# Optimization experiments

Hardware: AMD Instinct MI355X
Metric: run time of the kernel (lower is better)

Reference implementation:

```python
import jax, jax.numpy as jnp
import numpy as np

WS = 8                       # window size (square)
N = WS * WS                  # tokens per window
RES_H, RES_W = 32, 32        # input_resolution
DIM = 512
NUM_HEADS = 16
HEAD_DIM = DIM // NUM_HEADS
SCALE = HEAD_DIM ** -0.5
TABLE = 2 * WS - 1           # size of a_p/b_p/a_r/b_r tables
B_ = 1024                    # num_windows * batch


def _rel_coords():
    c = np.arange(WS)
    coords = np.stack(np.meshgrid(c, c, indexing='ij'))          # (2, WS, WS)
    cf = coords.reshape(2, -1)                                   # (2, N)
    rel = cf[:, :, None] - cf[:, None, :]                        # (2, N, N), values in [-(WS-1), WS-1]
    return rel[0], rel[1]                                        # radius (dh), azimuth (dw)

RADIUS_NP, AZIMUTH_NP = _rel_coords()
# torch indexes the (2*WS-1)-row tables with negative indices -> python wrap: -k maps to TABLE-k
IDX_R = jnp.asarray(RADIUS_NP % TABLE)
IDX_AZ = jnp.asarray(AZIMUTH_NP % TABLE)
RADIUS = jnp.asarray(RADIUS_NP, dtype=jnp.float32)               # (N, N)
AZIMUTH = jnp.asarray(AZIMUTH_NP, dtype=jnp.float32)             # (N, N)


def setup_inputs() -> dict:
    key = jax.random.key(0)
    ks = jax.random.split(key, 10)
    return {
        'x': jax.random.normal(ks[0], (B_, N, DIM), dtype=jnp.float32),
        'theta_max': jnp.ones((), dtype=jnp.float32) * 1.5708,   # ~pi/2 field-of-view half-angle
        'qkv_w': jax.random.normal(ks[1], (3 * DIM, DIM), dtype=jnp.float32) * 0.02,
        'qkv_b': jnp.zeros((3 * DIM,), dtype=jnp.float32),
        'proj_w': jax.random.normal(ks[2], (DIM, DIM), dtype=jnp.float32) * 0.02,
        'proj_b': jnp.zeros((DIM,), dtype=jnp.float32),
        'a_p': jax.random.normal(ks[3], (TABLE, NUM_HEADS), dtype=jnp.float32) * 0.02,
        'b_p': jax.random.normal(ks[4], (TABLE, NUM_HEADS), dtype=jnp.float32) * 0.02,
        'a_r': jax.random.normal(ks[5], (TABLE, NUM_HEADS), dtype=jnp.float32) * 0.02,
        'b_r': jax.random.normal(ks[6], (TABLE, NUM_HEADS), dtype=jnp.float32) * 0.02,
    }


def _trig_bias(table_a, table_b, idx, angle):
    # table_[ab]: (TABLE, H); idx: (N, N) int; angle: (N, N) float (possibly traced)
    a = table_a[idx]                                              # (N, N, H)
    b = table_b[idx]
    ang = angle[:, :, None]                                       # (N, N, 1)
    bias = a * jnp.cos(ang) + b * jnp.sin(ang)                    # (N, N, H)
    return jnp.transpose(bias, (2, 0, 1))                         # (H, N, N)


def reference(x, theta_max, qkv_w, qkv_b, proj_w, proj_b, a_p, b_p, a_r, b_r):
    Bw, n, c = x.shape
    qkv = x @ qkv_w.T + qkv_b                                     # (B_, N, 3*DIM)
    qkv = qkv.reshape(Bw, n, 3, NUM_HEADS, HEAD_DIM)
    qkv = jnp.transpose(qkv, (2, 0, 3, 1, 4))                     # (3, B_, H, N, hd)
    q, k, v = qkv[0] * SCALE, qkv[1], qkv[2]

    attn = jnp.einsum('bhid,bhjd->bhij', q, k)                    # (B_, H, N, N)

    az_angle = AZIMUTH * (2.0 * np.pi / RES_W)                    # (N, N)
    A_phi = _trig_bias(a_p, b_p, IDX_AZ, az_angle)                # (H, N, N)
    r_angle = RADIUS * (theta_max / RES_H)                        # (N, N), traced via theta_max
    A_theta = _trig_bias(a_r, b_r, IDX_R, r_angle)                # (H, N, N)

    attn = attn + A_phi[None] + A_theta[None]
    attn = jax.nn.softmax(attn, axis=-1)

    out = jnp.einsum('bhij,bhjd->bhid', attn, v)                  # (B_, H, N, hd)
    out = jnp.transpose(out, (0, 2, 1, 3)).reshape(Bw, n, c)      # (B_, N, DIM)
    out = out @ proj_w.T + proj_b
    return out
```

## Files before the change

### kernel.cpp

```cpp
#include <hip/hip_runtime.h>
#include <hip/hip_bf16.h>


typedef __bf16 bf16_t;
typedef bf16_t bf16x8 __attribute__((ext_vector_type(8)));
typedef float  f32x4  __attribute__((ext_vector_type(4)));

#define NWIN   1024
#define NTOK   64
#define DIM    512
#define NHEADS 16
#define HD     32
#define MTOT   (NWIN*NTOK)
#define QKVN   (3*DIM)
#define SCALE  0.17677669529663687f

__device__ __forceinline__ void async_copy16(const void* g, void* lds_generic) {
    __builtin_amdgcn_global_load_lds(
        (__attribute__((address_space(1))) unsigned int*)(unsigned long long)g,
        (__attribute__((address_space(3))) unsigned int*)(unsigned int)(unsigned long long)lds_generic,
        16, 0, 0);
}

__global__ void cvt_f32_bf16(const float* __restrict__ in, bf16_t* __restrict__ out, int n8) {
    int i = blockIdx.x * blockDim.x + threadIdx.x;
    if (i >= n8) return;
    const float4* p = (const float4*)in;
    float4 a = p[2*i], b = p[2*i+1];
    bf16x8 o;
    o[0]=(bf16_t)a.x; o[1]=(bf16_t)a.y; o[2]=(bf16_t)a.z; o[3]=(bf16_t)a.w;
    o[4]=(bf16_t)b.x; o[5]=(bf16_t)b.y; o[6]=(bf16_t)b.z; o[7]=(bf16_t)b.w;
    ((bf16x8*)out)[i] = o;
}

__global__ void bias_kernel(const float* __restrict__ ap, const float* __restrict__ bp,
                            const float* __restrict__ ar, const float* __restrict__ br,
                            const float* __restrict__ theta_max, float* __restrict__ bias) {
    int idx = blockIdx.x * 256 + threadIdx.x;
    int h  = idx >> 12;
    int ij = idx & 4095;
    int i = ij >> 6, j = ij & 63;
    int ri = i >> 3, ci = i & 7, rj = j >> 3, cj = j & 7;
    int rad = ri - rj, az = ci - cj;
    int idx_r  = rad < 0 ? rad + 15 : rad;
    int idx_az = az  < 0 ? az  + 15 : az;
    float azang = (float)az * 0.19634954084936207f;
    float rang  = (float)rad * (theta_max[0] * (1.0f/32.0f));
    float v = ap[idx_az*NHEADS + h] * cosf(azang) + bp[idx_az*NHEADS + h] * sinf(azang)
            + ar[idx_r *NHEADS + h] * cosf(rang)  + br[idx_r *NHEADS + h] * sinf(rang);
    bias[idx] = v;
}

template<int OUT_BF16>
__global__ __launch_bounds__(256, 2)
void gemm_bt(const bf16_t* __restrict__ A, const bf16_t* __restrict__ Bt,
             const float* __restrict__ bias, void* __restrict__ C,
             int M, int N, int K, int ntiles) {
    __shared__ bf16_t sA[128*64];
    __shared__ bf16_t sB[128*64];

    int bid = blockIdx.x;
    int bm = bid / ntiles, bn = bid % ntiles;
    int tid = threadIdx.x;
    int w = tid >> 6, lane = tid & 63;
    int quad = lane >> 4, l16 = lane & 15;
    int wm = w >> 1, wn = w & 1;

    f32x4 acc[4][4] = {};

    const bf16_t* Abase = A  + (size_t)(bm*128) * K;
    const bf16_t* Bbase = Bt + (size_t)(bn*128) * K;

    for (int k0 = 0; k0 < K; k0 += 64) {
        for (int i = 0; i < 4; ++i) {
            int off = w*4096 + i*1024 + lane*16;
            int r  = off >> 7;
            int pb = (off >> 4) & 7;
            int cb = pb ^ (r & 7);
            async_copy16(Abase + (size_t)r*K + k0 + cb*8, (char*)sA + w*4096 + i*1024);
            async_copy16(Bbase + (size_t)r*K + k0 + cb*8, (char*)sB + w*4096 + i*1024);
        }
        __syncthreads();

        for (int kk = 0; kk < 64; kk += 32) {
            bf16x8 af[4], bf[4];
            for (int mi = 0; mi < 4; ++mi) {
                int r  = wm*64 + mi*16 + l16;
                int cb = (kk >> 3) + quad;
                int pb = cb ^ (r & 7);
                af[mi] = *(const bf16x8*)((const char*)sA + r*128 + pb*16);
            }
            for (int ni = 0; ni < 4; ++ni) {
                int r  = wn*64 + ni*16 + l16;
                int cb = (kk >> 3) + quad;
                int pb = cb ^ (r & 7);
                bf[ni] = *(const bf16x8*)((const char*)sB + r*128 + pb*16);
            }
            for (int mi = 0; mi < 4; ++mi)
                for (int ni = 0; ni < 4; ++ni)
                    acc[mi][ni] = __builtin_amdgcn_mfma_f32_16x16x32_bf16(
                        af[mi], bf[ni], acc[mi][ni], 0, 0, 0);
        }
        __syncthreads();
    }

    for (int ni = 0; ni < 4; ++ni) {
        int col = bn*128 + wn*64 + ni*16 + l16;
        float bv = bias[col];
        for (int mi = 0; mi < 4; ++mi) {
            int row0 = bm*128 + wm*64 + mi*16 + quad*4;
            f32x4 a = acc[mi][ni];
            for (int reg = 0; reg < 4; ++reg) {
                float v = a[reg] + bv;
                size_t o = (size_t)(row0 + reg) * N + col;
                if (OUT_BF16) ((bf16_t*)C)[o] = (bf16_t)v;
                else          ((float*)C)[o]  = v;
            }
        }
    }
}

__global__ __launch_bounds__(256)
void attn_kernel(const bf16_t* __restrict__ qkv, const float* __restrict__ bias,
                 bf16_t* __restrict__ h2) {
    __shared__ bf16_t P[64*72];
    __shared__ bf16_t vT[32*64];

    int b = blockIdx.x >> 4, h = blockIdx.x & 15;
    int tid = threadIdx.x;
    int w = tid >> 6, lane = tid & 63, quad = lane >> 4, l16 = lane & 15;
    const bf16_t* base = qkv + (size_t)(b*64) * QKVN;

    {
        int t = tid & 63, dg = tid >> 6;
        bf16x8 vv = *(const bf16x8*)(base + (size_t)t*QKVN + 1024 + h*32 + dg*8);
        for (int j = 0; j < 8; ++j) vT[(dg*8 + j)*64 + t] = vv[j];
    }

    int m0 = w * 16;
    bf16x8 aq = *(const bf16x8*)(base + (size_t)(m0 + l16)*QKVN + h*32 + quad*8);
    f32x4 zero = {0.f, 0.f, 0.f, 0.f};
    f32x4 accS[4];
    for (int jt = 0; jt < 4; ++jt) {
        bf16x8 bk = *(const bf16x8*)(base + (size_t)(jt*16 + l16)*QKVN + 512 + h*32 + quad*8);
        accS[jt] = __builtin_amdgcn_mfma_f32_16x16x32_bf16(aq, bk, zero, 0, 0, 0);
    }

    const float* bh = bias + h*4096;
    float p[4][4], inv[4];
    for (int reg = 0; reg < 4; ++reg) {
        int row = m0 + quad*4 + reg;
        for (int jt = 0; jt < 4; ++jt)
            p[jt][reg] = accS[jt][reg] * SCALE + bh[row*64 + jt*16 + l16];
        float m = fmaxf(fmaxf(p[0][reg], p[1][reg]), fmaxf(p[2][reg], p[3][reg]));
        for (int off = 1; off < 16; off <<= 1) m = fmaxf(m, __shfl_xor(m, off));
        float s = 0.f;
        for (int jt = 0; jt < 4; ++jt) { p[jt][reg] = __expf(p[jt][reg] - m); s += p[jt][reg]; }
        for (int off = 1; off < 16; off <<= 1) s += __shfl_xor(s, off);
        inv[reg] = 1.0f / s;
    }
    for (int reg = 0; reg < 4; ++reg) {
        int row = m0 + quad*4 + reg;
        for (int jt = 0; jt < 4; ++jt)
            P[row*72 + jt*16 + l16] = (bf16_t)p[jt][reg];
    }
    __syncthreads();

    f32x4 accO[2] = {zero, zero};
    for (int kb = 0; kb < 64; kb += 32) {
        bf16x8 ap = *(const bf16x8*)(&P[(m0 + l16)*72 + kb + quad*8]);
        for (int nt = 0; nt < 2; ++nt) {
            bf16x8 bv = *(const bf16x8*)(&vT[(nt*16 + l16)*64 + kb + quad*8]);
            accO[nt] = __builtin_amdgcn_mfma_f32_16x16x32_bf16(ap, bv, accO[nt], 0, 0, 0);
        }
    }
    for (int nt = 0; nt < 2; ++nt) {
        for (int reg = 0; reg < 4; ++reg) {
            int row = b*64 + m0 + quad*4 + reg;
            int col = h*32 + nt*16 + l16;
            h2[(size_t)row*DIM + col] = (bf16_t)(accO[nt][reg] * inv[reg]);
        }
    }
}

extern "C" void kernel_launch(void* const* d_in, const int* in_sizes, int n_in,
                              void* d_out, int out_size, void* d_ws, size_t ws_size,
                              hipStream_t stream) {
    const float* x      = (const float*)d_in[0];
    const float* theta  = (const float*)d_in[1];
    const float* qkv_w  = (const float*)d_in[2];
    const float* qkv_b  = (const float*)d_in[3];
    const float* proj_w = (const float*)d_in[4];
    const float* proj_b = (const float*)d_in[5];
    const float* a_p    = (const float*)d_in[6];
    const float* b_p    = (const float*)d_in[7];
    const float* a_r    = (const float*)d_in[8];
    const float* b_r    = (const float*)d_in[9];
    float* out = (float*)d_out;

    char* ws = (char*)d_ws;
    bf16_t* qkvbuf = (bf16_t*)ws;
    bf16_t* xb     = (bf16_t*)(ws + 201326592);
    bf16_t* h2     = (bf16_t*)(ws + 201326592 + 67108864);
    bf16_t* wqkv   = (bf16_t*)(ws + 201326592 + 2*67108864);
    bf16_t* wproj  = (bf16_t*)(ws + 201326592 + 2*67108864 + 1572864);
    float*  biasbf = (float*) (ws + 201326592 + 2*67108864 + 1572864 + 524288);

    cvt_f32_bf16<<<(MTOT*DIM/8)/256, 256, 0, stream>>>(x, xb, MTOT*DIM/8);
    cvt_f32_bf16<<<(QKVN*DIM/8)/256, 256, 0, stream>>>(qkv_w, wqkv, QKVN*DIM/8);
    cvt_f32_bf16<<<(DIM*DIM/8)/256, 256, 0, stream>>>(proj_w, wproj, DIM*DIM/8);

    bias_kernel<<<256, 256, 0, stream>>>(a_p, b_p, a_r, b_r, theta, biasbf);

    gemm_bt<1><<<(MTOT/128)*(QKVN/128), 256, 0, stream>>>(xb, wqkv, qkv_b, qkvbuf,
                                                          MTOT, QKVN, DIM, QKVN/128);
    attn_kernel<<<NWIN*NHEADS, 256, 0, stream>>>(qkvbuf, biasbf, h2);

    gemm_bt<0><<<(MTOT/128)*(DIM/128), 256, 0, stream>>>(h2, wproj, proj_b, out,
                                                         MTOT, DIM, DIM, DIM/128);
}
```

Baseline: 558.2 us.

## Fuse per-window attention over all heads with output projection in one kernel

Replaces the per-(window,head) attention kernel and the separate projection GEMM with a single kernel per window. It loops over all 16 heads, accumulates the concatenated head outputs in LDS, then multiplies by the projection weights read directly from global memory and adds the bias. This removes the bf16 intermediate h2 round trip and one launch, but there are only 1024 blocks, heads run serially with barriers, and the proj weights are reloaded from global/L2 by every block without LDS staging.

```diff
diff --git a/kernel.cpp b/kernel.cpp
--- a/kernel.cpp
+++ b/kernel.cpp
@@ -120,65 +120,92 @@
     }
 }
 
-__global__ __launch_bounds__(256)
-void attn_kernel(const bf16_t* __restrict__ qkv, const float* __restrict__ bias,
-                 bf16_t* __restrict__ h2) {
+__global__ __launch_bounds__(256, 2)
+void attn_proj_kernel(const bf16_t* __restrict__ qkv, const float* __restrict__ bias,
+                      const bf16_t* __restrict__ projw, const float* __restrict__ projb,
+                      float* __restrict__ out) {
+    __shared__ bf16_t aout[64*520];
     __shared__ bf16_t P[64*72];
-    __shared__ bf16_t vT[32*64];
-
-    int b = blockIdx.x >> 4, h = blockIdx.x & 15;
+    __shared__ bf16_t vT[32*72];
+
+    int b = blockIdx.x;
     int tid = threadIdx.x;
     int w = tid >> 6, lane = tid & 63, quad = lane >> 4, l16 = lane & 15;
     const bf16_t* base = qkv + (size_t)(b*64) * QKVN;
-
-    {
-        int t = tid & 63, dg = tid >> 6;
-        bf16x8 vv = *(const bf16x8*)(base + (size_t)t*QKVN + 1024 + h*32 + dg*8);
-        for (int j = 0; j < 8; ++j) vT[(dg*8 + j)*64 + t] = vv[j];
-    }
-
+    f32x4 zero = {0.f, 0.f, 0.f, 0.f};
     int m0 = w * 16;
-    bf16x8 aq = *(const bf16x8*)(base + (size_t)(m0 + l16)*QKVN + h*32 + quad*8);
-    f32x4 zero = {0.f, 0.f, 0.f, 0.f};
-    f32x4 accS[4];
-    for (int jt = 0; jt < 4; ++jt) {
-        bf16x8 bk = *(const bf16x8*)(base + (size_t)(jt*16 + l16)*QKVN + 512 + h*32 + quad*8);
-        accS[jt] = __builtin_amdgcn_mfma_f32_16x16x32_bf16(aq, bk, zero, 0, 0, 0);
-    }
-
-    const float* bh = bias + h*4096;
-    float p[4][4], inv[4];
-    for (int reg = 0; reg < 4; ++reg) {
-        int row = m0 + quad*4 + reg;
-        for (int jt = 0; jt < 4; ++jt)
-            p[jt][reg] = accS[jt][reg] * SCALE + bh[row*64 + jt*16 + l16];
-        float m = fmaxf(fmaxf(p[0][reg], p[1][reg]), fmaxf(p[2][reg], p[3][reg]));
-        for (int off = 1; off < 16; off <<= 1) m = fmaxf(m, __shfl_xor(m, off));
-        float s = 0.f;
-        for (int jt = 0; jt < 4; ++jt) { p[jt][reg] = __expf(p[jt][reg] - m); s += p[jt][reg]; }
-        for (int off = 1; off < 16; off <<= 1) s += __shfl_xor(s, off);
-        inv[reg] = 1.0f / s;
-    }
-    for (int reg = 0; reg < 4; ++reg) {
-        int row = m0 + quad*4 + reg;
-        for (int jt = 0; jt < 4; ++jt)
-            P[row*72 + jt*16 + l16] = (bf16_t)p[jt][reg];
-    }
-    __syncthreads();
-
-    f32x4 accO[2] = {zero, zero};
-    for (int kb = 0; kb < 64; kb += 32) {
-        bf16x8 ap = *(const bf16x8*)(&P[(m0 + l16)*72 + kb + quad*8]);
-        for (int nt = 0; nt < 2; ++nt) {
-            bf16x8 bv = *(const bf16x8*)(&vT[(nt*16 + l16)*64 + kb + quad*8]);
-            accO[nt] = __builtin_amdgcn_mfma_f32_16x16x32_bf16(ap, bv, accO[nt], 0, 0, 0);
-        }
-    }
-    for (int nt = 0; nt < 2; ++nt) {
+
+    for (int h = 0; h < NHEADS; ++h) {
+        {
+            int t = tid & 63, dg = tid >> 6;
+            bf16x8 vv = *(const bf16x8*)(base + (size_t)t*QKVN + 1024 + h*32 + dg*8);
+            for (int j = 0; j < 8; ++j) vT[(dg*8 + j)*72 + t] = vv[j];
+        }
+
+        bf16x8 aq = *(const bf16x8*)(base + (size_t)(m0 + l16)*QKVN + h*32 + quad*8);
+        f32x4 accS[4];
+        for (int jt = 0; jt < 4; ++jt) {
+            bf16x8 bk = *(const bf16x8*)(base + (size_t)(jt*16 + l16)*QKVN + 512 + h*32 + quad*8);
+            accS[jt] = __builtin_amdgcn_mfma_f32_16x16x32_bf16(aq, bk, zero, 0, 0, 0);
+        }
+
+        const float* bh = bias + h*4096;
+        float p[4][4], inv[4];
         for (int reg = 0; reg < 4; ++reg) {
-            int row = b*64 + m0 + quad*4 + reg;
-            int col = h*32 + nt*16 + l16;
-            h2[(size_t)row*DIM + col] = (bf16_t)(accO[nt][reg] * inv[reg]);
+            int row = m0 + quad*4 + reg;
+            for (int jt = 0; jt < 4; ++jt)
+                p[jt][reg] = accS[jt][reg] * SCALE + bh[row*64 + jt*16 + l16];
+            float m = fmaxf(fmaxf(p[0][reg], p[1][reg]), fmaxf(p[2][reg], p[3][reg]));
+            for (int off = 1; off < 16; off <<= 1) m = fmaxf(m, __shfl_xor(m, off));
+            float s = 0.f;
+            for (int jt = 0; jt < 4; ++jt) { p[jt][reg] = __expf(p[jt][reg] - m); s += p[jt][reg]; }
+            for (int off = 1; off < 16; off <<= 1) s += __shfl_xor(s, off);
+            inv[reg] = 1.0f / s;
+        }
+        for (int reg = 0; reg < 4; ++reg) {
+            int row = m0 + quad*4 + reg;
+            for (int jt = 0; jt < 4; ++jt)
+                P[row*72 + jt*16 + l16] = (bf16_t)p[jt][reg];
+        }
+        __syncthreads();
+
+        f32x4 accO[2] = {zero, zero};
+        for (int kb = 0; kb < 64; kb += 32) {
+            bf16x8 ap = *(const bf16x8*)(&P[(m0 + l16)*72 + kb + quad*8]);
+            for (int nt = 0; nt < 2; ++nt) {
+                bf16x8 bv = *(const bf16x8*)(&vT[(nt*16 + l16)*72 + kb + quad*8]);
+                accO[nt] = __builtin_amdgcn_mfma_f32_16x16x32_bf16(ap, bv, accO[nt], 0, 0, 0);
+            }
+        }
+        for (int nt = 0; nt < 2; ++nt)
+            for (int reg = 0; reg < 4; ++reg)
+                aout[(m0 + quad*4 + reg)*520 + h*32 + nt*16 + l16] =
+                    (bf16_t)(accO[nt][reg] * inv[reg]);
+        __syncthreads();
+    }
+
+    for (int half = 0; half < 2; ++half) {
+        f32x4 acc[4][4] = {};
+        for (int kk = 0; kk < 512; kk += 32) {
+            bf16x8 af[4], bfr[4];
+            for (int mi = 0; mi < 4; ++mi)
+                af[mi] = *(const bf16x8*)(&aout[(mi*16 + l16)*520 + kk + quad*8]);
+            for (int ni = 0; ni < 4; ++ni)
+                bfr[ni] = *(const bf16x8*)(projw + (size_t)(w*128 + half*64 + ni*16 + l16)*512 + kk + quad*8);
+            for (int mi = 0; mi < 4; ++mi)
+                for (int ni = 0; ni < 4; ++ni)
+                    acc[mi][ni] = __builtin_amdgcn_mfma_f32_16x16x32_bf16(
+                        af[mi], bfr[ni], acc[mi][ni], 0, 0, 0);
+        }
+        for (int ni = 0; ni < 4; ++ni) {
+            int col = w*128 + half*64 + ni*16 + l16;
+            float bv = projb[col];
+            for (int mi = 0; mi < 4; ++mi) {
+                int row0 = b*64 + mi*16 + quad*4;
+                f32x4 a = acc[mi][ni];
+                for (int reg = 0; reg < 4; ++reg)
+                    out[(size_t)(row0 + reg)*DIM + col] = a[reg] + bv;
+            }
         }
     }
 }
@@ -201,10 +228,9 @@
     char* ws = (char*)d_ws;
     bf16_t* qkvbuf = (bf16_t*)ws;
     bf16_t* xb     = (bf16_t*)(ws + 201326592);
-    bf16_t* h2     = (bf16_t*)(ws + 201326592 + 67108864);
-    bf16_t* wqkv   = (bf16_t*)(ws + 201326592 + 2*67108864);
-    bf16_t* wproj  = (bf16_t*)(ws + 201326592 + 2*67108864 + 1572864);
-    float*  biasbf = (float*) (ws + 201326592 + 2*67108864 + 1572864 + 524288);
+    bf16_t* wqkv   = (bf16_t*)(ws + 201326592 + 67108864);
+    bf16_t* wproj  = (bf16_t*)(ws + 201326592 + 67108864 + 1572864);
+    float*  biasbf = (float*) (ws + 201326592 + 67108864 + 1572864 + 524288);
 
     cvt_f32_bf16<<<(MTOT*DIM/8)/256, 256, 0, stream>>>(x, xb, MTOT*DIM/8);
     cvt_f32_bf16<<<(QKVN*DIM/8)/256, 256, 0, stream>>>(qkv_w, wqkv, QKVN*DIM/8);
@@ -214,8 +240,5 @@
 
     gemm_bt<1><<<(MTOT/128)*(QKVN/128), 256, 0, stream>>>(xb, wqkv, qkv_b, qkvbuf,
                                                           MTOT, QKVN, DIM, QKVN/128);
-    attn_kernel<<<NWIN*NHEADS, 256, 0, stream>>>(qkvbuf, biasbf, h2);
-
-    gemm_bt<0><<<(MTOT/128)*(DIM/128), 256, 0, stream>>>(h2, wproj, proj_b, out,
-                                                         MTOT, DIM, DIM, DIM/128);
-}
+    attn_proj_kernel<<<NWIN, 256, 0, stream>>>(qkvbuf, biasbf, wproj, proj_b, out);
+}
```

After: 534.7 us. 1.04x faster.
